# Performance work log

Measured on AMD Instinct MI355X. Metric: run time of the kernel, lower is better.

## Reference

```python
import jax, jax.numpy as jnp
import numpy as np

N_NODES = 100000
N_EDGES = 1000000
D = 64
L = 4
N_GRAPHS = 1024
OUT_DIM = 16


def setup_inputs() -> dict:
    key = jax.random.key(0)
    ks = jax.random.split(key, 10)
    x = jax.random.normal(ks[0], (N_NODES, D), dtype=jnp.float32)
    edge_index = jax.random.randint(ks[1], (2, N_EDGES), 0, N_NODES, dtype=jnp.int32)
    batch = jnp.sort(jax.random.randint(ks[2], (N_NODES,), 0, N_GRAPHS, dtype=jnp.int32))
    s = 1.0 / np.sqrt(D)
    Wrel = jax.random.uniform(ks[3], (L, D, D), jnp.float32, -s, s)
    brel = jax.random.uniform(ks[4], (L, D), jnp.float32, -s, s)
    Wroot = jax.random.uniform(ks[5], (L, D, D), jnp.float32, -s, s)
    W1 = jax.random.uniform(ks[6], (D, D), jnp.float32, -s, s)
    b1 = jax.random.uniform(ks[7], (D,), jnp.float32, -s, s)
    W2 = jax.random.uniform(ks[8], (D, OUT_DIM), jnp.float32, -s, s)
    b2 = jax.random.uniform(ks[9], (OUT_DIM,), jnp.float32, -s, s)
    return {"x": x, "edge_index": edge_index, "batch": batch,
            "Wrel": Wrel, "brel": brel, "Wroot": Wroot,
            "W1": W1, "b1": b1, "W2": W2, "b2": b2}


def reference(x, edge_index, batch, Wrel, brel, Wroot, W1, b1, W2, b2):
    src, dst = edge_index[0], edge_index[1]
    h = x
    for l in range(L):
        # GraphConv(aggr='add'): out = lin_rel(sum_{j in N(i)} h_j) + lin_root(h_i)
        agg = jax.ops.segment_sum(h[src], dst, num_segments=N_NODES)  # [N, D]
        h = agg @ Wrel[l] + brel[l] + h @ Wroot[l]
        h = jax.nn.relu(h)  # dropout_p=0.0 -> identity
    # global_add_pool over batch index
    g = jax.ops.segment_sum(h, batch, num_segments=N_GRAPHS)  # [G, D]
    y = jax.nn.relu(g @ W1 + b1) @ W2 + b2  # graph classifier head
    return y
```

## Files before the change

kernel.cpp:

```cpp
#include <hip/hip_runtime.h>

#define N_NODES 100000
#define N_EDGES 1000000
#define DIM 64
#define N_GRAPHS 1024
#define OUT_DIM 16
#define NLAYERS 4

#define BN 64
#define NB 1563
#define BLOCK 256
#define NWAVES 4
#define RPW 16
#define SA 65
#define NGRP 12500

#define NBKT2 391
#define BCH 4096
#define NBLK1 245
#define SLACK 1800
#define EPB (N_EDGES + NBKT2 * SLACK)
#define SENTSRC N_NODES

typedef unsigned short ushort8_t __attribute__((ext_vector_type(8)));
typedef unsigned short ushort4_t __attribute__((ext_vector_type(4)));
typedef __bf16 bf16x8v __attribute__((ext_vector_type(8)));
typedef float f32x4v __attribute__((ext_vector_type(4)));

union bfu { ushort8_t u; bf16x8v b; };

__device__ __forceinline__ float b2f(unsigned short u) {
    union { unsigned int i; float f; } c;
    c.i = ((unsigned int)u) << 16;
    return c.f;
}
__device__ __forceinline__ unsigned short f2b(float f) {
    union { float f; unsigned int i; } c;
    c.f = f;
    return (unsigned short)((c.i + 0x7FFFu + ((c.i >> 16) & 1u)) >> 16);
}

__device__ __forceinline__ int blk_excl_scan_256(int v, int tid, int* tmp) {
    int lane = tid & 63, w = tid >> 6;
    int inc = v;
#pragma unroll
    for (int o = 1; o < 64; o <<= 1) { int u = __shfl_up(inc, o, 64); if (lane >= o) inc += u; }
    __syncthreads();
    if (lane == 63) tmp[w] = inc;
    __syncthreads();
    if (tid == 0) { int r = 0; for (int i = 0; i < 4; ++i) { int t2 = tmp[i]; tmp[i] = r; r += t2; } }
    __syncthreads();
    return inc - v + tmp[w];
}

__global__ __launch_bounds__(256) void prep_kernel(const int* __restrict__ dst,
                                                   int* __restrict__ hblk,
                                                   const float4* __restrict__ x,
                                                   ushort4* __restrict__ bf0,
                                                   ushort4* __restrict__ bf1,
                                                   float* __restrict__ g,
                                                   const float* __restrict__ Wrel,
                                                   const float* __restrict__ Wroot,
                                                   unsigned short* __restrict__ wT) {
    __shared__ int h[NBKT2];
    int tid = threadIdx.x;
    for (int i = tid; i < NBKT2; i += 256) h[i] = 0;
    __syncthreads();
    int e0 = blockIdx.x * BCH;
    int nloc = min(BCH, N_EDGES - e0);
    const int4* __restrict__ dst4 = reinterpret_cast<const int4*>(dst + e0);
    int n4l = nloc >> 2;
    for (int i = tid; i < n4l; i += 256) {
        int4 d4 = dst4[i];
        atomicAdd(&h[d4.x >> 8], 1); atomicAdd(&h[d4.y >> 8], 1);
        atomicAdd(&h[d4.z >> 8], 1); atomicAdd(&h[d4.w >> 8], 1);
    }

    const int n4 = N_NODES * (DIM / 4);
    for (int i = blockIdx.x * 256 + tid; i < n4; i += NBLK1 * 256) {
        float4 v = x[i];
        ushort4 b;
        b.x = f2b(v.x); b.y = f2b(v.y); b.z = f2b(v.z); b.w = f2b(v.w);
        bf0[i] = b;
    }
    const int g4 = N_GRAPHS * (DIM / 4);
    float4 z4 = make_float4(0.f, 0.f, 0.f, 0.f);
    for (int i = blockIdx.x * 256 + tid; i < g4; i += NBLK1 * 256)
        reinterpret_cast<float4*>(g)[i] = z4;
    const int wtot = NLAYERS * DIM * 2 * DIM;
    for (int i = blockIdx.x * 256 + tid; i < wtot; i += NBLK1 * 256) {
        int k = i & 127, n = (i >> 7) & 63, l = i >> 13;
        float v = (k < DIM) ? Wrel[l * DIM * DIM + k * DIM + n]
                            : Wroot[l * DIM * DIM + (k - DIM) * DIM + n];
        wT[i] = f2b(v);
    }
    if (blockIdx.x == 0 && tid < 32) {
        ushort4 z; z.x = 0; z.y = 0; z.z = 0; z.w = 0;
        if (tid < 16) bf0[(size_t)N_NODES * 16 + tid] = z;
        else          bf1[(size_t)N_NODES * 16 + (tid - 16)] = z;
    }
    __syncthreads();
    for (int i = tid; i < NBKT2; i += 256) hblk[(size_t)blockIdx.x * NBKT2 + i] = h[i];
}

__global__ __launch_bounds__(256) void colscan_kernel(int* __restrict__ hblk,
                                                      int* __restrict__ gsize) {
    __shared__ int tmp[4];
    int c = blockIdx.x, t = threadIdx.x;
    int i0 = 2 * t, i1 = 2 * t + 1;
    int a = (i0 < NBLK1) ? hblk[(size_t)i0 * NBKT2 + c] : 0;
    int b = (i1 < NBLK1) ? hblk[(size_t)i1 * NBKT2 + c] : 0;
    int s = blk_excl_scan_256(a + b, t, tmp);
    if (i0 < NBLK1) hblk[(size_t)i0 * NBKT2 + c] = s;
    if (i1 < NBLK1) hblk[(size_t)i1 * NBKT2 + c] = s + a;
    if (t == 255) gsize[c] = s + a + b;
}

__global__ __launch_bounds__(256) void scanb2_kernel(const int* __restrict__ gsize,
                                                     int* __restrict__ Abase,
                                                     int* __restrict__ Bbase) {
    __shared__ int tmp[4];
    int t = threadIdx.x;
    int c0 = 2 * t, c1 = 2 * t + 1;
    int a = (c0 < NBKT2) ? gsize[c0] : 0;
    int b = (c1 < NBKT2) ? gsize[c1] : 0;
    int s = blk_excl_scan_256(a + b, t, tmp);
    if (c0 < NBKT2) Abase[c0] = s;
    if (c1 < NBKT2) Abase[c1] = s + a;
    int a2 = (c0 < NBKT2) ? a + SLACK : 0;
    int b2 = (c1 < NBKT2) ? b + SLACK : 0;
    int s2 = blk_excl_scan_256(a2 + b2, t, tmp);
    if (c0 < NBKT2) Bbase[c0] = (s2 + 7) & ~7;
    if (c1 < NBKT2) Bbase[c1] = (s2 + a2 + 7) & ~7;
}

__global__ __launch_bounds__(256) void p1_kernel(const int* __restrict__ src,
                                                 const int* __restrict__ dst,
                                                 const int* __restrict__ Abase,
                                                 const int* __restrict__ hblk,
                                                 int* __restrict__ edgesA) {
    __shared__ int h[NBKT2], start[NBKT2], curb[NBKT2], resv[NBKT2], tmp[4];
    __shared__ int sortedv[BCH];
    __shared__ unsigned short sortedb[BCH];
    int tid = threadIdx.x;
    int e0 = blockIdx.x * BCH;
    int nloc = min(BCH, N_EDGES - e0);
    for (int i = tid; i < NBKT2; i += 256) h[i] = 0;
    __syncthreads();
    int myc[16], myv[16];
    const int4* __restrict__ src4 = reinterpret_cast<const int4*>(src + e0);
    const int4* __restrict__ dst4 = reinterpret_cast<const int4*>(dst + e0);
    const int n4l = nloc >> 2;
#pragma unroll
    for (int k4 = 0; k4 < 4; ++k4) {
        int i4 = k4 * 256 + tid;
        if (i4 < n4l) {
            int4 d = dst4[i4];
            int4 s = src4[i4];
            myc[k4 * 4 + 0] = d.x >> 8; myv[k4 * 4 + 0] = ((d.x & 255) << 17) | s.x;
            myc[k4 * 4 + 1] = d.y >> 8; myv[k4 * 4 + 1] = ((d.y & 255) << 17) | s.y;
            myc[k4 * 4 + 2] = d.z >> 8; myv[k4 * 4 + 2] = ((d.z & 255) << 17) | s.z;
            myc[k4 * 4 + 3] = d.w >> 8; myv[k4 * 4 + 3] = ((d.w & 255) << 17) | s.w;
            atomicAdd(&h[myc[k4 * 4 + 0]], 1);
            atomicAdd(&h[myc[k4 * 4 + 1]], 1);
            atomicAdd(&h[myc[k4 * 4 + 2]], 1);
            atomicAdd(&h[myc[k4 * 4 + 3]], 1);
        } else {
#pragma unroll
            for (int j = 0; j < 4; ++j) myc[k4 * 4 + j] = -1;
        }
    }
    __syncthreads();
    {
        int a = (2 * tid < NBKT2) ? h[2 * tid] : 0;
        int b = (2 * tid + 1 < NBKT2) ? h[2 * tid + 1] : 0;
        int s = blk_excl_scan_256(a + b, tid, tmp);
        if (2 * tid < NBKT2) start[2 * tid] = s;
        if (2 * tid + 1 < NBKT2) start[2 * tid + 1] = s + a;
    }
    __syncthreads();
    for (int i = tid; i < NBKT2; i += 256) curb[i] = start[i];
    __syncthreads();
#pragma unroll
    for (int k = 0; k < 16; ++k) if (myc[k] >= 0) {
        int r = atomicAdd(&curb[myc[k]], 1);
        sortedv[r] = myv[k];
        sortedb[r] = (unsigned short)myc[k];
    }
    __syncthreads();
    for (int i = tid; i < NBKT2; i += 256) resv[i] = hblk[(size_t)blockIdx.x * NBKT2 + i];
    __syncthreads();
    for (int i = tid; i < nloc; i += 256) {
        int c = sortedb[i];
        edgesA[Abase[c] + resv[c] + (i - start[c])] = sortedv[i];
    }
}

__global__ __launch_bounds__(256) void p2_kernel(const int* __restrict__ gsize,
                                                 const int* __restrict__ Abase,
                                                 const int* __restrict__ Bbase,
                                                 const int* __restrict__ edgesA,
                                                 int* __restrict__ edgesB,
                                                 int* __restrict__ rpS,
                                                 int* __restrict__ wend8) {
    __shared__ int cnt[256], off[256], pend[256], curx[256], tmp[4];
    int b = blockIdx.x, tid = threadIdx.x;
    int nb0 = b * 256;
    int nn = min(256, N_NODES - nb0);
    int ne = gsize[b];
    int abase = Abase[b], bbase = Bbase[b];
    cnt[tid] = 0;
    __syncthreads();
    for (int i = tid; i < ne; i += 256) atomicAdd(&cnt[edgesA[abase + i] >> 17], 1);
    __syncthreads();
    int c = cnt[tid];
    int c8 = (tid < nn) ? ((c + 7) & ~7) : 0;
    int o = blk_excl_scan_256(c8, tid, tmp);
    off[tid] = o; pend[tid] = o + c8; curx[tid] = bbase + o;
    __syncthreads();
    int gc = nn >> 3;
    if (tid < gc) {
        rpS[(nb0 >> 3) + tid] = bbase + off[tid * 8];
        wend8[(nb0 >> 3) + tid] = bbase + pend[tid * 8 + 7];
    }
    for (int i = tid; i < ne; i += 256) {
        int p = edgesA[abase + i];
        int dl = p >> 17;
        int pos = atomicAdd(&curx[dl], 1);
        edgesB[pos] = ((dl & 7) << 17) | (p & 0x1FFFF);
    }
    __syncthreads();
    if (tid < nn) {
        int pe = bbase + pend[tid];
        int sent = ((tid & 7) << 17) | SENTSRC;
        for (int pos = curx[tid]; pos < pe; ++pos) edgesB[pos] = sent;
    }
}

template <bool LAST>
__global__ __launch_bounds__(BLOCK) void layer_kernel(
    const ushort8_t* __restrict__ hbf_in, ushort8_t* __restrict__ hbf_out,
    const unsigned short* __restrict__ wT, const float* __restrict__ brel,
    const int* __restrict__ rpS, const int* __restrict__ wend8,
    const int* __restrict__ edges8,
    const int* __restrict__ batch, float* __restrict__ g) {
    __shared__ float agg_s[BN * SA];
    const int tid = threadIdx.x;
    const int lane = tid & 63;
    const int wave = __builtin_amdgcn_readfirstlane(tid >> 6);
    const int node0 = blockIdx.x * BN;
    const int nvalid = min(BN, N_NODES - node0);

#pragma unroll
    for (int r = 0; r < RPW; ++r) agg_s[(wave * RPW + r) * SA + lane] = 0.f;

    const int ml = lane & 15;
    const int kq = lane >> 4;
    const int mrow = wave * 16 + ml;
    const int nrow = min(node0 + mrow, N_NODES - 1);
    bfu af2, af3;
    af2.u = hbf_in[(size_t)nrow * 8 + kq];
    af3.u = hbf_in[(size_t)nrow * 8 + 4 + kq];
    float brv[4];
#pragma unroll
    for (int nt = 0; nt < 4; ++nt) brv[nt] = brel[nt * 16 + ml];

    {
        const int gg = blockIdx.x * 8 + wave * 2;
        if (gg < NGRP) {
            const int eb    = rpS[gg];
            const int mid   = rpS[gg + 1];
            const int end   = wend8[gg + 1];
            const int nch   = (end - eb) >> 3;
            const int midch = (mid - eb) >> 3;
            const int m = lane & 15;
            const int q = lane >> 4;
            const ushort4_t* __restrict__ h4 = (const ushort4_t*)hbf_in;
            const int rbase = wave * RPW;

            float a0 = 0.f, a1 = 0.f, a2 = 0.f, a3 = 0.f;
            int cur = -1;

#define FLUSHROW(ROW) { \
    float f0 = a0, f1 = a1, f2 = a2, f3 = a3; \
    f0 += __shfl_xor(f0, 16, 64); f1 += __shfl_xor(f1, 16, 64); \
    f2 += __shfl_xor(f2, 16, 64); f3 += __shfl_xor(f3, 16, 64); \
    f0 += __shfl_xor(f0, 32, 64); f1 += __shfl_xor(f1, 32, 64); \
    f2 += __shfl_xor(f2, 32, 64); f3 += __shfl_xor(f3, 32, 64); \
    if (lane < 16) { \
        float* p = &agg_s[(rbase + (ROW)) * SA + m * 4]; \
        p[0] = f0; p[1] = f1; p[2] = f2; p[3] = f3; } }

#define LDW(WA, WB, CC) { \
    WA = edges8[eb + min((CC) * 8 + q,     lmax)]; \
    WB = edges8[eb + min((CC) * 8 + q + 4, lmax)]; }
#define GTH(VA_, VB_, WA, WB) { \
    VA_ = h4[(unsigned)(((WA) & 0x1FFFF) * 16 + m)]; \
    VB_ = h4[(unsigned)(((WB) & 0x1FFFF) * 16 + m)]; }

#define ACCV(VA_, VB_) { \
    a0 += b2f(VA_[0]); a1 += b2f(VA_[1]); a2 += b2f(VA_[2]); a3 += b2f(VA_[3]); \
    a0 += b2f(VB_[0]); a1 += b2f(VB_[1]); a2 += b2f(VB_[2]); a3 += b2f(VB_[3]); }

#define STEP(U_, CC_) { \
    LDW(wA[((U_) + 6) & 7], wB[((U_) + 6) & 7], (CC_) + 6) \
    GTH(VA[((U_) + 3) & 3], VB[((U_) + 3) & 3], wA[((U_) + 3) & 7], wB[((U_) + 3) & 7]) \
    const int row_ = (__builtin_amdgcn_readfirstlane(wA[(U_) & 7]) >> 17) \
                     + (((CC_) >= midch) ? 8 : 0); \
    if (row_ != cur) { \
        if (cur >= 0) FLUSHROW(cur) \
        cur = row_; \
        a0 = a1 = a2 = a3 = 0.f; \
    } \
    ACCV(VA[(U_) & 3], VB[(U_) & 3]) }

            if (nch > 0) {
                const int lmax = nch * 8 - 1;
                int wA[8], wB[8];
                ushort4_t VA[4], VB[4];

#pragma unroll
                for (int p = 0; p < 6; ++p) LDW(wA[p], wB[p], p)
#pragma unroll
                for (int p = 0; p < 3; ++p) GTH(VA[p], VB[p], wA[p], wB[p])

                int c = 0;
                for (; c + 8 <= nch; c += 8) {
#pragma unroll
                    for (int u = 0; u < 8; ++u) STEP(u, c + u)
                }
                if (c < nch) {
#pragma unroll
                    for (int u = 0; u < 8; ++u) {
                        if (c + u < nch) STEP(u, c + u)
                    }
                }
                if (cur >= 0) FLUSHROW(cur)
            }
#undef STEP
#undef ACCV
#undef LDW
#undef GTH
#undef FLUSHROW
        }
    }
    __syncthreads();

    {
        bfu af[4];
#pragma unroll
        for (int kb = 0; kb < 2; ++kb) {
            const float* ap = &agg_s[mrow * SA + kb * 32 + kq * 8];
#pragma unroll
            for (int j = 0; j < 8; ++j) af[kb].u[j] = f2b(ap[j]);
        }
        af[2] = af2;
        af[3] = af3;

        f32x4v acc[4];
#pragma unroll
        for (int nt = 0; nt < 4; ++nt) {
            float bv = brv[nt];
            acc[nt][0] = bv; acc[nt][1] = bv; acc[nt][2] = bv; acc[nt][3] = bv;
        }
#pragma unroll
        for (int nt = 0; nt < 4; ++nt) {
            const ushort8_t* wrow =
                (const ushort8_t*)(wT + (size_t)(nt * 16 + ml) * 128);
#pragma unroll
            for (int kb = 0; kb < 4; ++kb) {
                bfu bfr; bfr.u = wrow[kb * 4 + kq];
                acc[nt] = __builtin_amdgcn_mfma_f32_16x16x32_bf16(
                    af[kb].b, bfr.b, acc[nt], 0, 0, 0);
            }
        }
        __syncthreads();
#pragma unroll
        for (int nt = 0; nt < 4; ++nt)
#pragma unroll
            for (int r = 0; r < 4; ++r)
                agg_s[(wave * 16 + kq * 4 + r) * SA + nt * 16 + ml] =
                    fmaxf(acc[nt][r], 0.f);
    }
    __syncthreads();

    if (LAST) {
        if (wave == 0) {
            float acc = 0.f;
            int cur = batch[node0];
            for (int nl = 0; nl < nvalid; ++nl) {
                int bv = batch[node0 + nl];
                float v = agg_s[nl * SA + lane];
                if (bv != cur) {
                    unsafeAtomicAdd(&g[(size_t)cur * DIM + lane], acc);
                    acc = 0.f; cur = bv;
                }
                acc += v;
            }
            unsafeAtomicAdd(&g[(size_t)cur * DIM + lane], acc);
        }
    } else {
        for (int i = tid; i < nvalid * 8; i += BLOCK) {
            int nl = i >> 3, c8 = i & 7;
            const float* xp = &agg_s[nl * SA + c8 * 8];
            ushort8_t b;
#pragma unroll
            for (int j = 0; j < 8; ++j) b[j] = f2b(xp[j]);
            hbf_out[(size_t)(node0 + nl) * 8 + c8] = b;
        }
    }
}

__global__ __launch_bounds__(256) void head_kernel(
    const float* __restrict__ g, const float* __restrict__ W1, const float* __restrict__ b1,
    const float* __restrict__ W2, const float* __restrict__ b2, float* __restrict__ y) {
    __shared__ float ts[4][DIM];
    const int wave = threadIdx.x >> 6, lane = threadIdx.x & 63;
    const int gid = blockIdx.x * 4 + wave;
    const float* __restrict__ grow = g + (size_t)gid * DIM;
    float t = b1[lane];
#pragma unroll 8
    for (int k = 0; k < DIM; ++k)
        t = fmaf(grow[k], W1[k * DIM + lane], t);
    ts[wave][lane] = fmaxf(t, 0.f);
    __syncthreads();
    if (lane < OUT_DIM) {
        float acc = b2[lane];
#pragma unroll 8
        for (int d = 0; d < DIM; ++d)
            acc = fmaf(ts[wave][d], W2[d * OUT_DIM + lane], acc);
        y[(size_t)gid * OUT_DIM + lane] = acc;
    }
}

extern "C" void kernel_launch(void* const* d_in, const int* in_sizes, int n_in,
                              void* d_out, int out_size, void* d_ws, size_t ws_size,
                              hipStream_t stream) {
    const float* x     = (const float*)d_in[0];
    const int*   eidx  = (const int*)d_in[1];
    const int*   batch = (const int*)d_in[2];
    const float* Wrel  = (const float*)d_in[3];
    const float* brel  = (const float*)d_in[4];
    const float* Wroot = (const float*)d_in[5];
    const float* W1    = (const float*)d_in[6];
    const float* b1    = (const float*)d_in[7];
    const float* W2    = (const float*)d_in[8];
    const float* b2    = (const float*)d_in[9];
    float* y = (float*)d_out;

    char* ws = (char*)d_ws;
    const size_t BFBYTES = (size_t)(N_NODES + 1) * DIM * sizeof(unsigned short);
    size_t off = 0;
    ushort4* bf0 = (ushort4*)(ws + off); off += (BFBYTES + 255) / 256 * 256;
    ushort4* bf1 = (ushort4*)(ws + off); off += (BFBYTES + 255) / 256 * 256;
    int* rpS    = (int*)(ws + off); off += (size_t)NGRP * 4;
    int* wend8  = (int*)(ws + off); off += (size_t)NGRP * 4;
    int* gsize  = (int*)(ws + off); off += (size_t)NBKT2 * 4;
    int* Abase  = (int*)(ws + off); off += (size_t)NBKT2 * 4;
    int* Bbase  = (int*)(ws + off); off += (size_t)NBKT2 * 4;
    int* hblk   = (int*)(ws + off); off += (size_t)NBLK1 * NBKT2 * 4;
    int* edgesA = (int*)(ws + off); off += (size_t)N_EDGES * 4;
    int* edgesB = (int*)(ws + off); off += (size_t)EPB * 4;
    float* g    = (float*)(ws + off); off += (size_t)N_GRAPHS * DIM * 4;
    unsigned short* wT = (unsigned short*)(ws + off);
    off += (size_t)NLAYERS * DIM * 2 * DIM * sizeof(unsigned short);

    const int* src = eidx;
    const int* dst = eidx + N_EDGES;

    prep_kernel<<<NBLK1, 256, 0, stream>>>(dst, hblk, (const float4*)x, bf0, bf1, g,
                                           Wrel, Wroot, wT);
    colscan_kernel<<<NBKT2, 256, 0, stream>>>(hblk, gsize);
    scanb2_kernel<<<1, 256, 0, stream>>>(gsize, Abase, Bbase);
    p1_kernel<<<NBLK1, 256, 0, stream>>>(src, dst, Abase, hblk, edgesA);
    p2_kernel<<<NBKT2, 256, 0, stream>>>(gsize, Abase, Bbase, edgesA, edgesB, rpS, wend8);

    layer_kernel<false><<<NB, BLOCK, 0, stream>>>((const ushort8_t*)bf0, (ushort8_t*)bf1,
        wT + 0 * DIM * 2 * DIM, brel + 0 * DIM, rpS, wend8, edgesB, batch, g);
    layer_kernel<false><<<NB, BLOCK, 0, stream>>>((const ushort8_t*)bf1, (ushort8_t*)bf0,
        wT + 1 * DIM * 2 * DIM, brel + 1 * DIM, rpS, wend8, edgesB, batch, g);
    layer_kernel<false><<<NB, BLOCK, 0, stream>>>((const ushort8_t*)bf0, (ushort8_t*)bf1,
        wT + 2 * DIM * 2 * DIM, brel + 2 * DIM, rpS, wend8, edgesB, batch, g);
    layer_kernel<true><<<NB, BLOCK, 0, stream>>>((const ushort8_t*)bf1, (ushort8_t*)bf0,
        wT + 3 * DIM * 2 * DIM, brel + 3 * DIM, rpS, wend8, edgesB, batch, g);

    head_kernel<<<N_GRAPHS / 4, 256, 0, stream>>>(g, W1, b1, W2, b2, y);
}
```

Baseline: 264.5 us.

## Fuse CSR build kernels into one cooperative kernel with grid syncs

Merges the five preprocessing kernels (histogram/convert, column scan, bucket scan, partition pass 1, pass 2) into a single cooperative launch of 391 blocks separated by grid.sync barriers. This is meant to remove four kernel launch boundaries and their drain/launch gaps. In exchange, grid-wide barriers add their own cost, and the grid must fit co-resident, which 391 blocks of 256 threads should satisfy on this device. Blocks beyond 245 sit idle during the histogram and partition phases.

```diff
diff --git a/kernel.cpp b/kernel.cpp
--- a/kernel.cpp
+++ b/kernel.cpp
@@ -1,4 +1,7 @@
 #include <hip/hip_runtime.h>
+#include <hip/hip_cooperative_groups.h>
+
+namespace cg = cooperative_groups;
 
 #define N_NODES 100000
 #define N_EDGES 1000000
@@ -53,187 +56,180 @@
     return inc - v + tmp[w];
 }
 
-__global__ __launch_bounds__(256) void prep_kernel(const int* __restrict__ dst,
-                                                   int* __restrict__ hblk,
-                                                   const float4* __restrict__ x,
-                                                   ushort4* __restrict__ bf0,
-                                                   ushort4* __restrict__ bf1,
-                                                   float* __restrict__ g,
-                                                   const float* __restrict__ Wrel,
-                                                   const float* __restrict__ Wroot,
-                                                   unsigned short* __restrict__ wT) {
-    __shared__ int h[NBKT2];
-    int tid = threadIdx.x;
-    for (int i = tid; i < NBKT2; i += 256) h[i] = 0;
-    __syncthreads();
-    int e0 = blockIdx.x * BCH;
-    int nloc = min(BCH, N_EDGES - e0);
-    const int4* __restrict__ dst4 = reinterpret_cast<const int4*>(dst + e0);
-    int n4l = nloc >> 2;
-    for (int i = tid; i < n4l; i += 256) {
-        int4 d4 = dst4[i];
-        atomicAdd(&h[d4.x >> 8], 1); atomicAdd(&h[d4.y >> 8], 1);
-        atomicAdd(&h[d4.z >> 8], 1); atomicAdd(&h[d4.w >> 8], 1);
-    }
-
-    const int n4 = N_NODES * (DIM / 4);
-    for (int i = blockIdx.x * 256 + tid; i < n4; i += NBLK1 * 256) {
-        float4 v = x[i];
-        ushort4 b;
-        b.x = f2b(v.x); b.y = f2b(v.y); b.z = f2b(v.z); b.w = f2b(v.w);
-        bf0[i] = b;
-    }
-    const int g4 = N_GRAPHS * (DIM / 4);
-    float4 z4 = make_float4(0.f, 0.f, 0.f, 0.f);
-    for (int i = blockIdx.x * 256 + tid; i < g4; i += NBLK1 * 256)
-        reinterpret_cast<float4*>(g)[i] = z4;
-    const int wtot = NLAYERS * DIM * 2 * DIM;
-    for (int i = blockIdx.x * 256 + tid; i < wtot; i += NBLK1 * 256) {
-        int k = i & 127, n = (i >> 7) & 63, l = i >> 13;
-        float v = (k < DIM) ? Wrel[l * DIM * DIM + k * DIM + n]
-                            : Wroot[l * DIM * DIM + (k - DIM) * DIM + n];
-        wT[i] = f2b(v);
-    }
-    if (blockIdx.x == 0 && tid < 32) {
-        ushort4 z; z.x = 0; z.y = 0; z.z = 0; z.w = 0;
-        if (tid < 16) bf0[(size_t)N_NODES * 16 + tid] = z;
-        else          bf1[(size_t)N_NODES * 16 + (tid - 16)] = z;
-    }
-    __syncthreads();
-    for (int i = tid; i < NBKT2; i += 256) hblk[(size_t)blockIdx.x * NBKT2 + i] = h[i];
-}
-
-__global__ __launch_bounds__(256) void colscan_kernel(int* __restrict__ hblk,
-                                                      int* __restrict__ gsize) {
-    __shared__ int tmp[4];
-    int c = blockIdx.x, t = threadIdx.x;
-    int i0 = 2 * t, i1 = 2 * t + 1;
-    int a = (i0 < NBLK1) ? hblk[(size_t)i0 * NBKT2 + c] : 0;
-    int b = (i1 < NBLK1) ? hblk[(size_t)i1 * NBKT2 + c] : 0;
-    int s = blk_excl_scan_256(a + b, t, tmp);
-    if (i0 < NBLK1) hblk[(size_t)i0 * NBKT2 + c] = s;
-    if (i1 < NBLK1) hblk[(size_t)i1 * NBKT2 + c] = s + a;
-    if (t == 255) gsize[c] = s + a + b;
-}
-
-__global__ __launch_bounds__(256) void scanb2_kernel(const int* __restrict__ gsize,
-                                                     int* __restrict__ Abase,
-                                                     int* __restrict__ Bbase) {
-    __shared__ int tmp[4];
-    int t = threadIdx.x;
-    int c0 = 2 * t, c1 = 2 * t + 1;
-    int a = (c0 < NBKT2) ? gsize[c0] : 0;
-    int b = (c1 < NBKT2) ? gsize[c1] : 0;
-    int s = blk_excl_scan_256(a + b, t, tmp);
-    if (c0 < NBKT2) Abase[c0] = s;
-    if (c1 < NBKT2) Abase[c1] = s + a;
-    int a2 = (c0 < NBKT2) ? a + SLACK : 0;
-    int b2 = (c1 < NBKT2) ? b + SLACK : 0;
-    int s2 = blk_excl_scan_256(a2 + b2, t, tmp);
-    if (c0 < NBKT2) Bbase[c0] = (s2 + 7) & ~7;
-    if (c1 < NBKT2) Bbase[c1] = (s2 + a2 + 7) & ~7;
-}
-
-__global__ __launch_bounds__(256) void p1_kernel(const int* __restrict__ src,
-                                                 const int* __restrict__ dst,
-                                                 const int* __restrict__ Abase,
-                                                 const int* __restrict__ hblk,
-                                                 int* __restrict__ edgesA) {
+__global__ __launch_bounds__(256) void build_kernel(
+    const int* __restrict__ src, const int* __restrict__ dst,
+    const float4* __restrict__ x,
+    int* __restrict__ hblk, ushort4* __restrict__ bf0, ushort4* __restrict__ bf1,
+    float* __restrict__ g, const float* __restrict__ Wrel,
+    const float* __restrict__ Wroot, unsigned short* __restrict__ wT,
+    int* __restrict__ gsize, int* __restrict__ Abase, int* __restrict__ Bbase,
+    int* __restrict__ edgesA, int* __restrict__ edgesB,
+    int* __restrict__ rpS, int* __restrict__ wend8) {
+    cg::grid_group grid = cg::this_grid();
     __shared__ int h[NBKT2], start[NBKT2], curb[NBKT2], resv[NBKT2], tmp[4];
     __shared__ int sortedv[BCH];
     __shared__ unsigned short sortedb[BCH];
-    int tid = threadIdx.x;
-    int e0 = blockIdx.x * BCH;
-    int nloc = min(BCH, N_EDGES - e0);
-    for (int i = tid; i < NBKT2; i += 256) h[i] = 0;
-    __syncthreads();
-    int myc[16], myv[16];
-    const int4* __restrict__ src4 = reinterpret_cast<const int4*>(src + e0);
-    const int4* __restrict__ dst4 = reinterpret_cast<const int4*>(dst + e0);
-    const int n4l = nloc >> 2;
-#pragma unroll
-    for (int k4 = 0; k4 < 4; ++k4) {
-        int i4 = k4 * 256 + tid;
-        if (i4 < n4l) {
-            int4 d = dst4[i4];
-            int4 s = src4[i4];
-            myc[k4 * 4 + 0] = d.x >> 8; myv[k4 * 4 + 0] = ((d.x & 255) << 17) | s.x;
-            myc[k4 * 4 + 1] = d.y >> 8; myv[k4 * 4 + 1] = ((d.y & 255) << 17) | s.y;
-            myc[k4 * 4 + 2] = d.z >> 8; myv[k4 * 4 + 2] = ((d.z & 255) << 17) | s.z;
-            myc[k4 * 4 + 3] = d.w >> 8; myv[k4 * 4 + 3] = ((d.w & 255) << 17) | s.w;
-            atomicAdd(&h[myc[k4 * 4 + 0]], 1);
-            atomicAdd(&h[myc[k4 * 4 + 1]], 1);
-            atomicAdd(&h[myc[k4 * 4 + 2]], 1);
-            atomicAdd(&h[myc[k4 * 4 + 3]], 1);
-        } else {
-#pragma unroll
-            for (int j = 0; j < 4; ++j) myc[k4 * 4 + j] = -1;
-        }
-    }
-    __syncthreads();
+    const int tid = threadIdx.x, bid = blockIdx.x;
+    const int GSTR = NBKT2 * 256;
+
+    if (bid < NBLK1) {
+        for (int i = tid; i < NBKT2; i += 256) h[i] = 0;
+        __syncthreads();
+        int e0 = bid * BCH;
+        int nloc = min(BCH, N_EDGES - e0);
+        const int4* __restrict__ dst4 = reinterpret_cast<const int4*>(dst + e0);
+        int n4l = nloc >> 2;
+        for (int i = tid; i < n4l; i += 256) {
+            int4 d4 = dst4[i];
+            atomicAdd(&h[d4.x >> 8], 1); atomicAdd(&h[d4.y >> 8], 1);
+            atomicAdd(&h[d4.z >> 8], 1); atomicAdd(&h[d4.w >> 8], 1);
+        }
+    }
     {
-        int a = (2 * tid < NBKT2) ? h[2 * tid] : 0;
-        int b = (2 * tid + 1 < NBKT2) ? h[2 * tid + 1] : 0;
+        const int n4 = N_NODES * (DIM / 4);
+        for (int i = bid * 256 + tid; i < n4; i += GSTR) {
+            float4 v = x[i];
+            ushort4 b;
+            b.x = f2b(v.x); b.y = f2b(v.y); b.z = f2b(v.z); b.w = f2b(v.w);
+            bf0[i] = b;
+        }
+        const int g4 = N_GRAPHS * (DIM / 4);
+        float4 z4 = make_float4(0.f, 0.f, 0.f, 0.f);
+        for (int i = bid * 256 + tid; i < g4; i += GSTR)
+            reinterpret_cast<float4*>(g)[i] = z4;
+        const int wtot = NLAYERS * DIM * 2 * DIM;
+        for (int i = bid * 256 + tid; i < wtot; i += GSTR) {
+            int k = i & 127, n = (i >> 7) & 63, l = i >> 13;
+            float v = (k < DIM) ? Wrel[l * DIM * DIM + k * DIM + n]
+                                : Wroot[l * DIM * DIM + (k - DIM) * DIM + n];
+            wT[i] = f2b(v);
+        }
+        if (bid == 0 && tid < 32) {
+            ushort4 z; z.x = 0; z.y = 0; z.z = 0; z.w = 0;
+            if (tid < 16) bf0[(size_t)N_NODES * 16 + tid] = z;
+            else          bf1[(size_t)N_NODES * 16 + (tid - 16)] = z;
+        }
+    }
+    if (bid < NBLK1) {
+        __syncthreads();
+        for (int i = tid; i < NBKT2; i += 256) hblk[(size_t)bid * NBKT2 + i] = h[i];
+    }
+    grid.sync();
+
+    {
+        int c = bid;
+        int i0 = 2 * tid, i1 = 2 * tid + 1;
+        int a = (i0 < NBLK1) ? hblk[(size_t)i0 * NBKT2 + c] : 0;
+        int b = (i1 < NBLK1) ? hblk[(size_t)i1 * NBKT2 + c] : 0;
         int s = blk_excl_scan_256(a + b, tid, tmp);
-        if (2 * tid < NBKT2) start[2 * tid] = s;
-        if (2 * tid + 1 < NBKT2) start[2 * tid + 1] = s + a;
-    }
-    __syncthreads();
-    for (int i = tid; i < NBKT2; i += 256) curb[i] = start[i];
-    __syncthreads();
-#pragma unroll
-    for (int k = 0; k < 16; ++k) if (myc[k] >= 0) {
-        int r = atomicAdd(&curb[myc[k]], 1);
-        sortedv[r] = myv[k];
-        sortedb[r] = (unsigned short)myc[k];
-    }
-    __syncthreads();
-    for (int i = tid; i < NBKT2; i += 256) resv[i] = hblk[(size_t)blockIdx.x * NBKT2 + i];
-    __syncthreads();
-    for (int i = tid; i < nloc; i += 256) {
-        int c = sortedb[i];
-        edgesA[Abase[c] + resv[c] + (i - start[c])] = sortedv[i];
-    }
-}
-
-__global__ __launch_bounds__(256) void p2_kernel(const int* __restrict__ gsize,
-                                                 const int* __restrict__ Abase,
-                                                 const int* __restrict__ Bbase,
-                                                 const int* __restrict__ edgesA,
-                                                 int* __restrict__ edgesB,
-                                                 int* __restrict__ rpS,
-                                                 int* __restrict__ wend8) {
-    __shared__ int cnt[256], off[256], pend[256], curx[256], tmp[4];
-    int b = blockIdx.x, tid = threadIdx.x;
-    int nb0 = b * 256;
-    int nn = min(256, N_NODES - nb0);
-    int ne = gsize[b];
-    int abase = Abase[b], bbase = Bbase[b];
-    cnt[tid] = 0;
-    __syncthreads();
-    for (int i = tid; i < ne; i += 256) atomicAdd(&cnt[edgesA[abase + i] >> 17], 1);
-    __syncthreads();
-    int c = cnt[tid];
-    int c8 = (tid < nn) ? ((c + 7) & ~7) : 0;
-    int o = blk_excl_scan_256(c8, tid, tmp);
-    off[tid] = o; pend[tid] = o + c8; curx[tid] = bbase + o;
-    __syncthreads();
-    int gc = nn >> 3;
-    if (tid < gc) {
-        rpS[(nb0 >> 3) + tid] = bbase + off[tid * 8];
-        wend8[(nb0 >> 3) + tid] = bbase + pend[tid * 8 + 7];
-    }
-    for (int i = tid; i < ne; i += 256) {
-        int p = edgesA[abase + i];
-        int dl = p >> 17;
-        int pos = atomicAdd(&curx[dl], 1);
-        edgesB[pos] = ((dl & 7) << 17) | (p & 0x1FFFF);
-    }
-    __syncthreads();
-    if (tid < nn) {
-        int pe = bbase + pend[tid];
-        int sent = ((tid & 7) << 17) | SENTSRC;
-        for (int pos = curx[tid]; pos < pe; ++pos) edgesB[pos] = sent;
+        if (i0 < NBLK1) hblk[(size_t)i0 * NBKT2 + c] = s;
+        if (i1 < NBLK1) hblk[(size_t)i1 * NBKT2 + c] = s + a;
+        if (tid == 255) gsize[c] = s + a + b;
+    }
+    grid.sync();
+
+    if (bid == 0) {
+        int c0 = 2 * tid, c1 = 2 * tid + 1;
+        int a = (c0 < NBKT2) ? gsize[c0] : 0;
+        int b = (c1 < NBKT2) ? gsize[c1] : 0;
+        int s = blk_excl_scan_256(a + b, tid, tmp);
+        if (c0 < NBKT2) Abase[c0] = s;
+        if (c1 < NBKT2) Abase[c1] = s + a;
+        int a2 = (c0 < NBKT2) ? a + SLACK : 0;
+        int b2 = (c1 < NBKT2) ? b + SLACK : 0;
+        int s2 = blk_excl_scan_256(a2 + b2, tid, tmp);
+        if (c0 < NBKT2) Bbase[c0] = (s2 + 7) & ~7;
+        if (c1 < NBKT2) Bbase[c1] = (s2 + a2 + 7) & ~7;
+    }
+    grid.sync();
+
+    if (bid < NBLK1) {
+        int e0 = bid * BCH;
+        int nloc = min(BCH, N_EDGES - e0);
+        for (int i = tid; i < NBKT2; i += 256) h[i] = 0;
+        __syncthreads();
+        int myc[16], myv[16];
+        const int4* __restrict__ src4 = reinterpret_cast<const int4*>(src + e0);
+        const int4* __restrict__ dst4 = reinterpret_cast<const int4*>(dst + e0);
+        const int n4l = nloc >> 2;
+#pragma unroll
+        for (int k4 = 0; k4 < 4; ++k4) {
+            int i4 = k4 * 256 + tid;
+            if (i4 < n4l) {
+                int4 d = dst4[i4];
+                int4 s = src4[i4];
+                myc[k4 * 4 + 0] = d.x >> 8; myv[k4 * 4 + 0] = ((d.x & 255) << 17) | s.x;
+                myc[k4 * 4 + 1] = d.y >> 8; myv[k4 * 4 + 1] = ((d.y & 255) << 17) | s.y;
+                myc[k4 * 4 + 2] = d.z >> 8; myv[k4 * 4 + 2] = ((d.z & 255) << 17) | s.z;
+                myc[k4 * 4 + 3] = d.w >> 8; myv[k4 * 4 + 3] = ((d.w & 255) << 17) | s.w;
+                atomicAdd(&h[myc[k4 * 4 + 0]], 1);
+                atomicAdd(&h[myc[k4 * 4 + 1]], 1);
+                atomicAdd(&h[myc[k4 * 4 + 2]], 1);
+                atomicAdd(&h[myc[k4 * 4 + 3]], 1);
+            } else {
+#pragma unroll
+                for (int j = 0; j < 4; ++j) myc[k4 * 4 + j] = -1;
+            }
+        }
+        __syncthreads();
+        {
+            int a = (2 * tid < NBKT2) ? h[2 * tid] : 0;
+            int b = (2 * tid + 1 < NBKT2) ? h[2 * tid + 1] : 0;
+            int s = blk_excl_scan_256(a + b, tid, tmp);
+            if (2 * tid < NBKT2) start[2 * tid] = s;
+            if (2 * tid + 1 < NBKT2) start[2 * tid + 1] = s + a;
+        }
+        __syncthreads();
+        for (int i = tid; i < NBKT2; i += 256) curb[i] = start[i];
+        __syncthreads();
+#pragma unroll
+        for (int k = 0; k < 16; ++k) if (myc[k] >= 0) {
+            int r = atomicAdd(&curb[myc[k]], 1);
+            sortedv[r] = myv[k];
+            sortedb[r] = (unsigned short)myc[k];
+        }
+        __syncthreads();
+        for (int i = tid; i < NBKT2; i += 256) resv[i] = hblk[(size_t)bid * NBKT2 + i];
+        __syncthreads();
+        for (int i = tid; i < nloc; i += 256) {
+            int c = sortedb[i];
+            edgesA[Abase[c] + resv[c] + (i - start[c])] = sortedv[i];
+        }
+    }
+    grid.sync();
+
+    {
+        int b = bid;
+        int nb0 = b * 256;
+        int nn = min(256, N_NODES - nb0);
+        int ne = gsize[b];
+        int abase = Abase[b], bbase = Bbase[b];
+        h[tid] = 0;
+        __syncthreads();
+        for (int i = tid; i < ne; i += 256) atomicAdd(&h[edgesA[abase + i] >> 17], 1);
+        __syncthreads();
+        int c = h[tid];
+        int c8 = (tid < nn) ? ((c + 7) & ~7) : 0;
+        int o = blk_excl_scan_256(c8, tid, tmp);
+        start[tid] = o; curb[tid] = o + c8; resv[tid] = bbase + o;
+        __syncthreads();
+        int gc = nn >> 3;
+        if (tid < gc) {
+            rpS[(nb0 >> 3) + tid] = bbase + start[tid * 8];
+            wend8[(nb0 >> 3) + tid] = bbase + curb[tid * 8 + 7];
+        }
+        for (int i = tid; i < ne; i += 256) {
+            int p = edgesA[abase + i];
+            int dl = p >> 17;
+            int pos = atomicAdd(&resv[dl], 1);
+            edgesB[pos] = ((dl & 7) << 17) | (p & 0x1FFFF);
+        }
+        __syncthreads();
+        if (tid < nn) {
+            int pe = bbase + curb[tid];
+            int sent = ((tid & 7) << 17) | SENTSRC;
+            for (int pos = resv[tid]; pos < pe; ++pos) edgesB[pos] = sent;
+        }
     }
 }
 
@@ -467,13 +463,17 @@
 
     const int* src = eidx;
     const int* dst = eidx + N_EDGES;
-
-    prep_kernel<<<NBLK1, 256, 0, stream>>>(dst, hblk, (const float4*)x, bf0, bf1, g,
-                                           Wrel, Wroot, wT);
-    colscan_kernel<<<NBKT2, 256, 0, stream>>>(hblk, gsize);
-    scanb2_kernel<<<1, 256, 0, stream>>>(gsize, Abase, Bbase);
-    p1_kernel<<<NBLK1, 256, 0, stream>>>(src, dst, Abase, hblk, edgesA);
-    p2_kernel<<<NBKT2, 256, 0, stream>>>(gsize, Abase, Bbase, edgesA, edgesB, rpS, wend8);
+    const float4* x4 = (const float4*)x;
+
+    void* kargs[] = {
+        (void*)&src, (void*)&dst, (void*)&x4,
+        (void*)&hblk, (void*)&bf0, (void*)&bf1, (void*)&g,
+        (void*)&Wrel, (void*)&Wroot, (void*)&wT,
+        (void*)&gsize, (void*)&Abase, (void*)&Bbase,
+        (void*)&edgesA, (void*)&edgesB, (void*)&rpS, (void*)&wend8
+    };
+    hipLaunchCooperativeKernel((void*)build_kernel, dim3(NBKT2), dim3(256),
+                               kargs, 0, stream);
 
     layer_kernel<false><<<NB, BLOCK, 0, stream>>>((const ushort8_t*)bf0, (ushort8_t*)bf1,
         wT + 0 * DIM * 2 * DIM, brel + 0 * DIM, rpS, wend8, edgesB, batch, g);
```

New measurement: 483.0 us. 1.83x slower.
